# Performance work log

Hardware: AMD Instinct MI355X
Metric: run time of the kernel (lower is better)

## Reference

```python
import jax, jax.numpy as jnp
import numpy as np
import math

NINP = 1024
NOUT = 1024
NSLOTS = 15
B = 4096


def setup_inputs() -> dict:
    key = jax.random.key(0)
    ks = jax.random.split(key, 10)
    inp = {
        "input": jax.random.normal(ks[0], (B, NINP), jnp.float32),
        "gate_time": jax.random.uniform(ks[1], (B, NSLOTS), jnp.float32),
        "rmask": jnp.ones((B, NOUT), jnp.float32),
        "memory_h": jax.random.normal(ks[2], (B, NSLOTS, NOUT), jnp.float32),
        "memory_c": jax.random.normal(ks[3], (B, NSLOTS, NOUT), jnp.float32),
        # projector_summ: Linear(ninp+nout, nout) (dropouts are identity in eval)
        "W_proj": jax.random.normal(ks[4], (NOUT, NINP + NOUT), jnp.float32) / np.sqrt(NINP + NOUT),
        "b_proj": jnp.zeros((NOUT,), jnp.float32),
        # LSTMCell(ninp, nout) weights, torch gate order [i, f, g, o]
        "W_ih": jax.random.normal(ks[5], (4 * NOUT, NINP), jnp.float32) / np.sqrt(NINP),
        "W_hh": jax.random.normal(ks[6], (4 * NOUT, NOUT), jnp.float32) / np.sqrt(NOUT),
        "b_ih": jnp.zeros((4 * NOUT,), jnp.float32),
        "b_hh": jnp.zeros((4 * NOUT,), jnp.float32),
    }
    return inp


def reference(input, gate_time, rmask, memory_h, memory_c,
              W_proj, b_proj, W_ih, W_hh, b_ih, b_hh):
    # --- attention over memory slots (gated softmax) ---
    key = jnp.concatenate([input, memory_h[:, 0, :]], axis=1) @ W_proj.T + b_proj  # [B, nout]
    logits = jnp.einsum('bsd,bd->bs', memory_h, key) / math.sqrt(NOUT)             # [B, nslots]
    e = jnp.exp(logits - jnp.max(logits, axis=1, keepdims=True)) * gate_time
    attention = e / jnp.sum(e, axis=1, keepdims=True)
    sel_h = jnp.einsum('bs,bsd->bd', attention, memory_h)
    sel_c = jnp.einsum('bs,bsd->bd', attention, memory_c)

    # --- LSTM cell step (dropout = identity in eval) ---
    gates = input @ W_ih.T + b_ih + (sel_h * rmask) @ W_hh.T + b_hh
    i, f, g, o = jnp.split(gates, 4, axis=1)
    c_i = jax.nn.sigmoid(f) * sel_c + jax.nn.sigmoid(i) * jnp.tanh(g)
    h_i = jax.nn.sigmoid(o) * jnp.tanh(c_i)

    # --- rolling memory update: push new state to slot 0 ---
    memory_h_new = jnp.concatenate([h_i[:, None, :], memory_h[:, :-1, :]], axis=1)
    memory_c_new = jnp.concatenate([c_i[:, None, :], memory_c[:, :-1, :]], axis=1)
    return h_i, memory_h_new, memory_c_new, attention
```

## Files before the change

kernel.cpp:

```cpp
#include <hip/hip_runtime.h>

typedef __attribute__((ext_vector_type(8))) __bf16 bf16x8;
typedef __attribute__((ext_vector_type(4))) float f32x4;
typedef unsigned short u16;
typedef unsigned int u32;

#define NINP 1024
#define NOUT 1024
#define NSLOTS 15
#define BB 4096

__device__ __forceinline__ u16 f2bf(float x) {
  u32 u = __float_as_uint(x);
  u = (u + 0x7FFFu + ((u >> 16) & 1u)) >> 16;
  return (u16)u;
}
__device__ __forceinline__ float bf2f(u16 u) {
  return __uint_as_float(((u32)u) << 16);
}
__device__ __forceinline__ float sigf(float x) {
  return 1.0f / (1.0f + __expf(-x));
}
__device__ __forceinline__ float tanhfast(float x) {
  return 1.0f - 2.0f / (__expf(2.0f * x) + 1.0f);
}

__device__ __forceinline__ void llds16(const u16* g, const u16* l) {
  __builtin_amdgcn_global_load_lds(
      (const __attribute__((address_space(1))) void*)g,
      (__attribute__((address_space(3))) void*)l, 16, 0, 0);
}

__global__ void convert_kernel(const float* __restrict__ input,
                               const float* __restrict__ mem_h,
                               const float* __restrict__ W_proj,
                               const float* __restrict__ W_ih,
                               const float* __restrict__ W_hh,
                               u16* __restrict__ X2, u16* __restrict__ WP,
                               u16* __restrict__ WG) {
  const int S0 = 4194304, S1 = 4194304, S2 = 2097152, S3 = 4194304, S4 = 4194304;
  const int total4 = (S0 + S1 + S2 + S3 + S4) >> 2;
  for (int i4 = blockIdx.x * blockDim.x + threadIdx.x; i4 < total4;
       i4 += gridDim.x * blockDim.x) {
    int i = i4 << 2;
    const float* src;
    u16* dst;
    if (i < S0) {
      int j = i, b = j >> 10, d = j & 1023;
      src = input + j;
      dst = X2 + ((size_t)b << 11) + d;
    } else if (i < S0 + S1) {
      int j = i - S0, b = j >> 10, d = j & 1023;
      src = mem_h + (size_t)b * (NSLOTS * NOUT) + d;
      dst = X2 + ((size_t)b << 11) + 1024 + d;
    } else if (i < S0 + S1 + S2) {
      int j = i - S0 - S1;
      src = W_proj + j;
      dst = WP + j;
    } else if (i < S0 + S1 + S2 + S3) {
      int j = i - S0 - S1 - S2, n = j >> 10, k = j & 1023;
      src = W_ih + j;
      dst = WG + ((size_t)n << 11) + k;
    } else {
      int j = i - S0 - S1 - S2 - S3, n = j >> 10, k = j & 1023;
      src = W_hh + j;
      dst = WG + ((size_t)n << 11) + 1024 + k;
    }
    float4 v = *(const float4*)src;
    ushort4 o;
    o.x = f2bf(v.x); o.y = f2bf(v.y); o.z = f2bf(v.z); o.w = f2bf(v.w);
    *(ushort4*)dst = o;
  }
}

__global__ __launch_bounds__(256) void gemm_bt(
    const u16* __restrict__ A, const u16* __restrict__ W,
    const float* __restrict__ bias1, const float* __restrict__ bias2,
    float* __restrict__ Cf, u16* __restrict__ Cb, int M, int N, int K) {
  __shared__ u16 sA[2][128 * 32];
  __shared__ u16 sB[2][128 * 32];
  const int t = threadIdx.x;
  const int wave = t >> 6, lane = t & 63;
  const int m0 = blockIdx.y * 128, n0 = blockIdx.x * 128;
  const int wr = (wave >> 1) * 64, wc = (wave & 1) * 64;

  f32x4 acc[4][4] = {};

  const int row0 = t >> 2, col0 = (t & 3) * 8;
  const int row1 = (t + 256) >> 2;
  const u16* Ag0 = A + (size_t)(m0 + row0) * K + col0;
  const u16* Ag1 = A + (size_t)(m0 + row1) * K + col0;
  const u16* Wg0 = W + (size_t)(n0 + row0) * K + col0;
  const u16* Wg1 = W + (size_t)(n0 + row1) * K + col0;
  const int l0 = (wave * 64) * 8;
  const int l1 = (256 + wave * 64) * 8;

  auto stage = [&](int buf, int kt) {
    const int k0 = kt * 32;
    llds16(Ag0 + k0, &sA[buf][l0]);
    llds16(Ag1 + k0, &sA[buf][l1]);
    llds16(Wg0 + k0, &sB[buf][l0]);
    llds16(Wg1 + k0, &sB[buf][l1]);
  };

  const int lrow = lane & 15;
  const int kq = (lane >> 4) * 8;

  const int nk = K / 32;
  stage(0, 0);
  for (int kt = 0; kt < nk; ++kt) {
    __syncthreads();
    if (kt + 1 < nk) stage((kt + 1) & 1, kt + 1);
    const int buf = kt & 1;
    bf16x8 af[4], bfr[4];
#pragma unroll
    for (int mi = 0; mi < 4; ++mi)
      af[mi] = *(const bf16x8*)&sA[buf][(wr + mi * 16 + lrow) * 32 + kq];
#pragma unroll
    for (int ni = 0; ni < 4; ++ni)
      bfr[ni] = *(const bf16x8*)&sB[buf][(wc + ni * 16 + lrow) * 32 + kq];
#pragma unroll
    for (int mi = 0; mi < 4; ++mi)
#pragma unroll
      for (int ni = 0; ni < 4; ++ni)
        acc[mi][ni] = __builtin_amdgcn_mfma_f32_16x16x32_bf16(
            af[mi], bfr[ni], acc[mi][ni], 0, 0, 0);
  }

  const int crow = (lane >> 4) * 4;
  const int ccol = lane & 15;
#pragma unroll
  for (int mi = 0; mi < 4; ++mi) {
#pragma unroll
    for (int ni = 0; ni < 4; ++ni) {
      int row = m0 + wr + mi * 16 + crow;
      int col = n0 + wc + ni * 16 + ccol;
      float bv = bias1 ? bias1[col] : 0.0f;
      if (bias2) bv += bias2[col];
#pragma unroll
      for (int r = 0; r < 4; ++r) {
        float v = acc[mi][ni][r] + bv;
        if (Cb)
          Cb[(size_t)(row + r) * N + col] = f2bf(v);
        else
          Cf[(size_t)(row + r) * N + col] = v;
      }
    }
  }
}

__global__ __launch_bounds__(512, 2) void gemm256(
    const u16* __restrict__ A, const u16* __restrict__ W,
    const float* __restrict__ bias1, const float* __restrict__ bias2,
    u16* __restrict__ Cb, int M, int N, int K) {
  extern __shared__ __align__(16) u16 smem[];
  u16* sA = smem;
  u16* sB = smem + 32768;

  const int t = threadIdx.x;
  const int wid = t >> 6, lane = t & 63;
  const int nbx = N >> 8;
  const int nb = (M >> 8) * nbx;
  const int cpx = nb >> 3;
  const int bid = blockIdx.x;
  const int wg = (bid & 7) * cpx + (bid >> 3);
  const int m0 = (wg / nbx) << 8;
  const int n0 = (wg % nbx) << 8;

  const int wm = wid >> 2, wn = wid & 3;

  f32x4 acc[8][4] = {};

  const int src_swz = ((lane >> 5) & 1) << 4;
  const u16* gA[4];
  const u16* gB[4];
#pragma unroll
  for (int j = 0; j < 4; ++j) {
    int row = (j & 1) * 128 + (t >> 2);
    int col = (j >> 1) * 32 + ((((t & 3) * 8) ^ src_swz));
    gA[j] = A + (size_t)(m0 + row) * K + col;
    gB[j] = W + (size_t)(n0 + row) * K + col;
  }
  auto stage = [&](int kt, int buf) {
    const int ko = kt * 64;
    const int lb = buf * 16384;
#pragma unroll
    for (int j = 0; j < 4; ++j)
      llds16(gA[j] + ko, sA + lb + (j * 512 + wid * 64) * 8);
#pragma unroll
    for (int j = 0; j < 4; ++j)
      llds16(gB[j] + ko, sB + lb + (j * 512 + wid * 64) * 8);
  };

  const int lrow = lane & 15;
  const int lcol = ((lane >> 4) * 8) ^ (((lane >> 3) & 1) << 4);
  const u16* pA = sA + (wm * 128 + lrow) * 32 + lcol;
  const u16* pB = sB + (wn * 64 + lrow) * 32 + lcol;

  const int NKT = K >> 6;
  stage(0, 0);
  for (int kt = 0; kt < NKT; ++kt) {
    const int buf = kt & 1;
    if (kt + 1 < NKT) {
      stage(kt + 1, buf ^ 1);
      asm volatile("s_waitcnt vmcnt(8)" ::: "memory");
      __builtin_amdgcn_sched_barrier(0);
    } else {
      asm volatile("s_waitcnt vmcnt(0)" ::: "memory");
      __builtin_amdgcn_sched_barrier(0);
    }
    __builtin_amdgcn_s_barrier();

    const u16* bA = pA + buf * 16384;
    const u16* bB = pB + buf * 16384;

    bf16x8 bf[4][2];
#pragma unroll
    for (int ni = 0; ni < 4; ++ni)
#pragma unroll
      for (int ks = 0; ks < 2; ++ks)
        bf[ni][ks] = *(const bf16x8*)(bB + ks * 8192 + ni * (16 * 32));

#pragma unroll
    for (int ph = 0; ph < 4; ++ph) {
      bf16x8 af[2][2];
#pragma unroll
      for (int m2 = 0; m2 < 2; ++m2)
#pragma unroll
        for (int ks = 0; ks < 2; ++ks)
          af[m2][ks] =
              *(const bf16x8*)(bA + ks * 8192 + (ph * 2 + m2) * (16 * 32));
      __builtin_amdgcn_s_setprio(1);
#pragma unroll
      for (int ks = 0; ks < 2; ++ks)
#pragma unroll
        for (int m2 = 0; m2 < 2; ++m2)
#pragma unroll
          for (int ni = 0; ni < 4; ++ni)
            acc[ph * 2 + m2][ni] = __builtin_amdgcn_mfma_f32_16x16x32_bf16(
                af[m2][ks], bf[ni][ks], acc[ph * 2 + m2][ni], 0, 0, 0);
      __builtin_amdgcn_s_setprio(0);
      __builtin_amdgcn_s_barrier();
    }
  }

  const int crow = (lane >> 4) * 4;
  const int ccol = lane & 15;
#pragma unroll
  for (int mi = 0; mi < 8; ++mi) {
#pragma unroll
    for (int ni = 0; ni < 4; ++ni) {
      int row = m0 + wm * 128 + mi * 16 + crow;
      int col = n0 + wn * 64 + ni * 16 + ccol;
      float bv = bias1[col] + bias2[col];
#pragma unroll
      for (int r = 0; r < 4; ++r)
        Cb[(size_t)(row + r) * N + col] = f2bf(acc[mi][ni][r] + bv);
    }
  }
}

__global__ __launch_bounds__(256) void attn_kernel(
    const float* __restrict__ mem_h, const float* __restrict__ mem_c,
    const float* __restrict__ key, const float* __restrict__ gate_time,
    const float* __restrict__ rmask, float* __restrict__ out_mh,
    float* __restrict__ out_mc, float* __restrict__ out_att,
    u16* __restrict__ X2, float* __restrict__ selc) {
  const int b = blockIdx.x;
  const int t = threadIdx.x;
  const int lane = t & 63, wave = t >> 6;

  const float4* mh4 = (const float4*)(mem_h + (size_t)b * (NSLOTS * NOUT));
  const float4* mc4 = (const float4*)(mem_c + (size_t)b * (NSLOTS * NOUT));
  float4 key4 = ((const float4*)(key + ((size_t)b << 10)))[t];

  float4 h[NSLOTS];
  float lg[NSLOTS];
#pragma unroll
  for (int s = 0; s < NSLOTS; ++s) {
    h[s] = mh4[s * 256 + t];
    lg[s] = h[s].x * key4.x + h[s].y * key4.y + h[s].z * key4.z + h[s].w * key4.w;
  }

  __shared__ float red[NSLOTS][4];
#pragma unroll
  for (int s = 0; s < NSLOTS; ++s) {
    float v = lg[s];
    v += __shfl_xor(v, 32); v += __shfl_xor(v, 16); v += __shfl_xor(v, 8);
    v += __shfl_xor(v, 4);  v += __shfl_xor(v, 2);  v += __shfl_xor(v, 1);
    if (lane == 0) red[s][wave] = v;
  }
  __syncthreads();

  float att[NSLOTS];
  float mx = -1e30f;
#pragma unroll
  for (int s = 0; s < NSLOTS; ++s) {
    float v = red[s][0] + red[s][1] + red[s][2] + red[s][3];
    att[s] = v * 0.03125f;
    mx = fmaxf(mx, att[s]);
  }
  float ssum = 0.0f;
#pragma unroll
  for (int s = 0; s < NSLOTS; ++s) {
    att[s] = __expf(att[s] - mx) * gate_time[b * NSLOTS + s];
    ssum += att[s];
  }
  float inv = 1.0f / ssum;
#pragma unroll
  for (int s = 0; s < NSLOTS; ++s) att[s] *= inv;
  if (t == 0) {
#pragma unroll
    for (int s = 0; s < NSLOTS; ++s) out_att[(size_t)b * NSLOTS + s] = att[s];
  }

  float4 sh = {0, 0, 0, 0};
  float4* omh = (float4*)(out_mh + (size_t)b * (NSLOTS * NOUT));
#pragma unroll
  for (int s = 0; s < NSLOTS; ++s) {
    sh.x += att[s] * h[s].x; sh.y += att[s] * h[s].y;
    sh.z += att[s] * h[s].z; sh.w += att[s] * h[s].w;
    if (s < NSLOTS - 1) omh[(s + 1) * 256 + t] = h[s];
  }
  float4 rm = ((const float4*)(rmask + ((size_t)b << 10)))[t];
  sh.x *= rm.x; sh.y *= rm.y; sh.z *= rm.z; sh.w *= rm.w;
  ushort4 shb;
  shb.x = f2bf(sh.x); shb.y = f2bf(sh.y); shb.z = f2bf(sh.z); shb.w = f2bf(sh.w);
  ((ushort4*)(X2 + ((size_t)b << 11) + 1024))[t] = shb;

  float4 sc = {0, 0, 0, 0};
  float4* omc = (float4*)(out_mc + (size_t)b * (NSLOTS * NOUT));
#pragma unroll
  for (int s = 0; s < NSLOTS; ++s) {
    float4 c = mc4[s * 256 + t];
    sc.x += att[s] * c.x; sc.y += att[s] * c.y;
    sc.z += att[s] * c.z; sc.w += att[s] * c.w;
    if (s < NSLOTS - 1) omc[(s + 1) * 256 + t] = c;
  }
  ((float4*)(selc + ((size_t)b << 10)))[t] = sc;
}

__global__ __launch_bounds__(256) void lstm_ew(const u16* __restrict__ gates,
                                               const float* __restrict__ selc,
                                               float* __restrict__ out_h,
                                               float* __restrict__ out_mh,
                                               float* __restrict__ out_mc) {
  int gid = blockIdx.x * blockDim.x + threadIdx.x;
  int b = gid >> 8, t = gid & 255;
  const ushort4* g = (const ushort4*)(gates + ((size_t)b << 12));
  ushort4 iu = g[t], fu = g[256 + t], gu = g[512 + t], ou = g[768 + t];
  float4 sc = ((const float4*)(selc + ((size_t)b << 10)))[t];

  float4 cv, hv;
  {
    float i0 = sigf(bf2f(iu.x)), f0 = sigf(bf2f(fu.x));
    float g0 = tanhfast(bf2f(gu.x)), o0 = sigf(bf2f(ou.x));
    cv.x = f0 * sc.x + i0 * g0; hv.x = o0 * tanhfast(cv.x);
  }
  {
    float i0 = sigf(bf2f(iu.y)), f0 = sigf(bf2f(fu.y));
    float g0 = tanhfast(bf2f(gu.y)), o0 = sigf(bf2f(ou.y));
    cv.y = f0 * sc.y + i0 * g0; hv.y = o0 * tanhfast(cv.y);
  }
  {
    float i0 = sigf(bf2f(iu.z)), f0 = sigf(bf2f(fu.z));
    float g0 = tanhfast(bf2f(gu.z)), o0 = sigf(bf2f(ou.z));
    cv.z = f0 * sc.z + i0 * g0; hv.z = o0 * tanhfast(cv.z);
  }
  {
    float i0 = sigf(bf2f(iu.w)), f0 = sigf(bf2f(fu.w));
    float g0 = tanhfast(bf2f(gu.w)), o0 = sigf(bf2f(ou.w));
    cv.w = f0 * sc.w + i0 * g0; hv.w = o0 * tanhfast(cv.w);
  }
  ((float4*)(out_h + ((size_t)b << 10)))[t] = hv;
  ((float4*)(out_mh + (size_t)b * (NSLOTS * NOUT)))[t] = hv;
  ((float4*)(out_mc + (size_t)b * (NSLOTS * NOUT)))[t] = cv;
}

extern "C" void kernel_launch(void* const* d_in, const int* in_sizes, int n_in,
                              void* d_out, int out_size, void* d_ws,
                              size_t ws_size, hipStream_t stream) {
  const float* input = (const float*)d_in[0];
  const float* gate_time = (const float*)d_in[1];
  const float* rmask = (const float*)d_in[2];
  const float* mem_h = (const float*)d_in[3];
  const float* mem_c = (const float*)d_in[4];
  const float* W_proj = (const float*)d_in[5];
  const float* b_proj = (const float*)d_in[6];
  const float* W_ih = (const float*)d_in[7];
  const float* W_hh = (const float*)d_in[8];
  const float* b_ih = (const float*)d_in[9];
  const float* b_hh = (const float*)d_in[10];

  float* out = (float*)d_out;
  float* out_h = out;
  float* out_mh = out + 4194304;
  float* out_mc = out_mh + 62914560;
  float* out_att = out_mc + 62914560;

  char* ws = (char*)d_ws;
  u16* X2 = (u16*)ws;
  u16* WP = (u16*)(ws + 16777216);
  u16* WG = (u16*)(ws + 20971520);
  float* key = (float*)(ws + 37748736);
  float* selc = (float*)(ws + 54525952);
  u16* gates = (u16*)(ws + 71303168);

  (void)hipFuncSetAttribute((const void*)gemm256,
                            hipFuncAttributeMaxDynamicSharedMemorySize, 131072);

  convert_kernel<<<2048, 256, 0, stream>>>(input, mem_h, W_proj, W_ih, W_hh, X2,
                                           WP, WG);
  gemm_bt<<<dim3(8, 32), 256, 0, stream>>>(X2, WP, b_proj, nullptr, key,
                                           nullptr, 4096, 1024, 2048);
  attn_kernel<<<4096, 256, 0, stream>>>(mem_h, mem_c, key, gate_time, rmask,
                                        out_mh, out_mc, out_att, X2, selc);
  gemm256<<<256, 512, 131072, stream>>>(X2, WG, b_ih, b_hh, gates, 4096, 4096,
                                        2048);
  lstm_ew<<<4096, 256, 0, stream>>>(gates, selc, out_h, out_mh, out_mc);
}
```

Before: 368.9 us.

## Fuse LSTM elementwise into gate GEMM epilogue with interleaved gate weight rows

Weight rows for the four LSTM gates are interleaved during conversion, so each 256-wide GEMM output tile holds all four gates for 64 hidden units. The GEMM epilogue stages accumulators through shared memory and computes the LSTM cell directly, writing h and c. This removes the bf16 gates buffer round trip and the separate lstm_ew launch. The projection GEMM also writes its key output in bf16 instead of fp32, which halves that traffic but adds rounding error to the attention logits.

```diff
diff --git a/kernel.cpp b/kernel.cpp
--- a/kernel.cpp
+++ b/kernel.cpp
@@ -59,12 +59,14 @@
       dst = WP + j;
     } else if (i < S0 + S1 + S2 + S3) {
       int j = i - S0 - S1 - S2, n = j >> 10, k = j & 1023;
+      int gate = n >> 10, d = n & 1023;
       src = W_ih + j;
-      dst = WG + ((size_t)n << 11) + k;
+      dst = WG + ((size_t)((d << 2) | gate) << 11) + k;
     } else {
       int j = i - S0 - S1 - S2 - S3, n = j >> 10, k = j & 1023;
+      int gate = n >> 10, d = n & 1023;
       src = W_hh + j;
-      dst = WG + ((size_t)n << 11) + 1024 + k;
+      dst = WG + ((size_t)((d << 2) | gate) << 11) + 1024 + k;
     }
     float4 v = *(const float4*)src;
     ushort4 o;
@@ -75,8 +77,8 @@
 
 __global__ __launch_bounds__(256) void gemm_bt(
     const u16* __restrict__ A, const u16* __restrict__ W,
-    const float* __restrict__ bias1, const float* __restrict__ bias2,
-    float* __restrict__ Cf, u16* __restrict__ Cb, int M, int N, int K) {
+    const float* __restrict__ bias1, u16* __restrict__ Cb, int M, int N,
+    int K) {
   __shared__ u16 sA[2][128 * 32];
   __shared__ u16 sB[2][128 * 32];
   const int t = threadIdx.x;
@@ -136,23 +138,19 @@
       int row = m0 + wr + mi * 16 + crow;
       int col = n0 + wc + ni * 16 + ccol;
       float bv = bias1 ? bias1[col] : 0.0f;
-      if (bias2) bv += bias2[col];
-#pragma unroll
-      for (int r = 0; r < 4; ++r) {
-        float v = acc[mi][ni][r] + bv;
-        if (Cb)
-          Cb[(size_t)(row + r) * N + col] = f2bf(v);
-        else
-          Cf[(size_t)(row + r) * N + col] = v;
-      }
-    }
-  }
-}
-
-__global__ __launch_bounds__(512, 2) void gemm256(
+#pragma unroll
+      for (int r = 0; r < 4; ++r)
+        Cb[(size_t)(row + r) * N + col] = f2bf(acc[mi][ni][r] + bv);
+    }
+  }
+}
+
+__global__ __launch_bounds__(512, 2) void gemm256_lstm(
     const u16* __restrict__ A, const u16* __restrict__ W,
-    const float* __restrict__ bias1, const float* __restrict__ bias2,
-    u16* __restrict__ Cb, int M, int N, int K) {
+    const float* __restrict__ b_ih, const float* __restrict__ b_hh,
+    const float* __restrict__ selc, float* __restrict__ out_h,
+    float* __restrict__ out_mh, float* __restrict__ out_mc, int M, int N,
+    int K) {
   extern __shared__ __align__(16) u16 smem[];
   u16* sA = smem;
   u16* sB = smem + 32768;
@@ -244,25 +242,64 @@
     }
   }
 
+  float* slab = (float*)smem;
   const int crow = (lane >> 4) * 4;
   const int ccol = lane & 15;
-#pragma unroll
+  const int d0 = n0 >> 2;
+
+  __builtin_amdgcn_s_barrier();
+#pragma unroll 1
   for (int mi = 0; mi < 8; ++mi) {
 #pragma unroll
     for (int ni = 0; ni < 4; ++ni) {
-      int row = m0 + wm * 128 + mi * 16 + crow;
-      int col = n0 + wn * 64 + ni * 16 + ccol;
-      float bv = bias1[col] + bias2[col];
+      int c = wn * 64 + ni * 16 + ccol;
+      int g = c & 3, dl = c >> 2;
 #pragma unroll
       for (int r = 0; r < 4; ++r)
-        Cb[(size_t)(row + r) * N + col] = f2bf(acc[mi][ni][r] + bv);
-    }
+        slab[wm * 4352 + (crow + r) * 272 + g * 68 + dl] = acc[mi][ni][r];
+    }
+    __builtin_amdgcn_s_barrier();
+    {
+      const int row_id = t >> 4;
+      const int slabi = row_id >> 4, rr = row_id & 15;
+      const int k4 = (t & 15) * 4;
+      const int grow = m0 + slabi * 128 + mi * 16 + rr;
+      const int gd = d0 + k4;
+      f32x4 gv[4];
+#pragma unroll
+      for (int g = 0; g < 4; ++g) {
+        f32x4 v = *(const f32x4*)&slab[slabi * 4352 + rr * 272 + g * 68 + k4];
+        float4 b1 = *(const float4*)&b_ih[(g << 10) + gd];
+        float4 b2 = *(const float4*)&b_hh[(g << 10) + gd];
+        gv[g][0] = v[0] + b1.x + b2.x;
+        gv[g][1] = v[1] + b1.y + b2.y;
+        gv[g][2] = v[2] + b1.z + b2.z;
+        gv[g][3] = v[3] + b1.w + b2.w;
+      }
+      float4 sc = *(const float4*)&selc[(size_t)grow * 1024 + gd];
+      float scv[4] = {sc.x, sc.y, sc.z, sc.w};
+      float4 cv, hv;
+      float cvv[4], hvv[4];
+#pragma unroll
+      for (int j = 0; j < 4; ++j) {
+        float ii = sigf(gv[0][j]), ff = sigf(gv[1][j]);
+        float gg = tanhfast(gv[2][j]), oo = sigf(gv[3][j]);
+        cvv[j] = ff * scv[j] + ii * gg;
+        hvv[j] = oo * tanhfast(cvv[j]);
+      }
+      cv.x = cvv[0]; cv.y = cvv[1]; cv.z = cvv[2]; cv.w = cvv[3];
+      hv.x = hvv[0]; hv.y = hvv[1]; hv.z = hvv[2]; hv.w = hvv[3];
+      *(float4*)&out_h[(size_t)grow * 1024 + gd] = hv;
+      *(float4*)&out_mh[(size_t)grow * (NSLOTS * NOUT) + gd] = hv;
+      *(float4*)&out_mc[(size_t)grow * (NSLOTS * NOUT) + gd] = cv;
+    }
+    __builtin_amdgcn_s_barrier();
   }
 }
 
 __global__ __launch_bounds__(256) void attn_kernel(
     const float* __restrict__ mem_h, const float* __restrict__ mem_c,
-    const float* __restrict__ key, const float* __restrict__ gate_time,
+    const u16* __restrict__ keyb, const float* __restrict__ gate_time,
     const float* __restrict__ rmask, float* __restrict__ out_mh,
     float* __restrict__ out_mc, float* __restrict__ out_att,
     u16* __restrict__ X2, float* __restrict__ selc) {
@@ -272,7 +309,8 @@
 
   const float4* mh4 = (const float4*)(mem_h + (size_t)b * (NSLOTS * NOUT));
   const float4* mc4 = (const float4*)(mem_c + (size_t)b * (NSLOTS * NOUT));
-  float4 key4 = ((const float4*)(key + ((size_t)b << 10)))[t];
+  ushort4 kb = ((const ushort4*)(keyb + ((size_t)b << 10)))[t];
+  float4 key4 = {bf2f(kb.x), bf2f(kb.y), bf2f(kb.z), bf2f(kb.w)};
 
   float4 h[NSLOTS];
   float lg[NSLOTS];
@@ -338,43 +376,6 @@
     if (s < NSLOTS - 1) omc[(s + 1) * 256 + t] = c;
   }
   ((float4*)(selc + ((size_t)b << 10)))[t] = sc;
-}
-
-__global__ __launch_bounds__(256) void lstm_ew(const u16* __restrict__ gates,
-                                               const float* __restrict__ selc,
-                                               float* __restrict__ out_h,
-                                               float* __restrict__ out_mh,
-                                               float* __restrict__ out_mc) {
-  int gid = blockIdx.x * blockDim.x + threadIdx.x;
-  int b = gid >> 8, t = gid & 255;
-  const ushort4* g = (const ushort4*)(gates + ((size_t)b << 12));
-  ushort4 iu = g[t], fu = g[256 + t], gu = g[512 + t], ou = g[768 + t];
-  float4 sc = ((const float4*)(selc + ((size_t)b << 10)))[t];
-
-  float4 cv, hv;
-  {
-    float i0 = sigf(bf2f(iu.x)), f0 = sigf(bf2f(fu.x));
-    float g0 = tanhfast(bf2f(gu.x)), o0 = sigf(bf2f(ou.x));
-    cv.x = f0 * sc.x + i0 * g0; hv.x = o0 * tanhfast(cv.x);
-  }
-  {
-    float i0 = sigf(bf2f(iu.y)), f0 = sigf(bf2f(fu.y));
-    float g0 = tanhfast(bf2f(gu.y)), o0 = sigf(bf2f(ou.y));
-    cv.y = f0 * sc.y + i0 * g0; hv.y = o0 * tanhfast(cv.y);
-  }
-  {
-    float i0 = sigf(bf2f(iu.z)), f0 = sigf(bf2f(fu.z));
-    float g0 = tanhfast(bf2f(gu.z)), o0 = sigf(bf2f(ou.z));
-    cv.z = f0 * sc.z + i0 * g0; hv.z = o0 * tanhfast(cv.z);
-  }
-  {
-    float i0 = sigf(bf2f(iu.w)), f0 = sigf(bf2f(fu.w));
-    float g0 = tanhfast(bf2f(gu.w)), o0 = sigf(bf2f(ou.w));
-    cv.w = f0 * sc.w + i0 * g0; hv.w = o0 * tanhfast(cv.w);
-  }
-  ((float4*)(out_h + ((size_t)b << 10)))[t] = hv;
-  ((float4*)(out_mh + (size_t)b * (NSLOTS * NOUT)))[t] = hv;
-  ((float4*)(out_mc + (size_t)b * (NSLOTS * NOUT)))[t] = cv;
 }
 
 extern "C" void kernel_launch(void* const* d_in, const int* in_sizes, int n_in,
@@ -402,20 +403,18 @@
   u16* X2 = (u16*)ws;
   u16* WP = (u16*)(ws + 16777216);
   u16* WG = (u16*)(ws + 20971520);
-  float* key = (float*)(ws + 37748736);
-  float* selc = (float*)(ws + 54525952);
-  u16* gates = (u16*)(ws + 71303168);
-
-  (void)hipFuncSetAttribute((const void*)gemm256,
+  u16* keyb = (u16*)(ws + 37748736);
+  float* selc = (float*)(ws + 46137344);
+
+  (void)hipFuncSetAttribute((const void*)gemm256_lstm,
                             hipFuncAttributeMaxDynamicSharedMemorySize, 131072);
 
   convert_kernel<<<2048, 256, 0, stream>>>(input, mem_h, W_proj, W_ih, W_hh, X2,
                                            WP, WG);
-  gemm_bt<<<dim3(8, 32), 256, 0, stream>>>(X2, WP, b_proj, nullptr, key,
-                                           nullptr, 4096, 1024, 2048);
-  attn_kernel<<<4096, 256, 0, stream>>>(mem_h, mem_c, key, gate_time, rmask,
+  gemm_bt<<<dim3(8, 32), 256, 0, stream>>>(X2, WP, b_proj, keyb, 4096, 1024,
+                                           2048);
+  attn_kernel<<<4096, 256, 0, stream>>>(mem_h, mem_c, keyb, gate_time, rmask,
                                         out_mh, out_mc, out_att, X2, selc);
-  gemm256<<<256, 512, 131072, stream>>>(X2, WG, b_ih, b_hh, gates, 4096, 4096,
-                                        2048);
-  lstm_ew<<<4096, 256, 0, stream>>>(gates, selc, out_h, out_mh, out_mc);
-}
+  gemm256_lstm<<<256, 512, 131072, stream>>>(X2, WG, b_ih, b_hh, selc, out_h,
+                                             out_mh, out_mc, 4096, 4096, 2048);
+}
```

After: 384.8 us. +4.3%, slower.

## Store key and selected cell state in bf16, use nontemporal streaming memory ops

Applied to the files above, without the earlier changes.

The projection GEMM now writes its key output in bf16 instead of fp32, and the attention kernel writes the attention-weighted cell state (selc) in bf16. This halves those intermediate buffers. The large memory_h/memory_c reads and shifted-slot writes switch to nontemporal loads and stores to avoid polluting cache, and the LSTM elementwise kernel processes 8 elements per thread with nontemporal stores. Keeping key and sel_c in bf16 adds precision loss to the logits and the cell-state path, which may hurt output accuracy.

```diff
diff --git a/kernel.cpp b/kernel.cpp
--- a/kernel.cpp
+++ b/kernel.cpp
@@ -2,6 +2,7 @@
 
 typedef __attribute__((ext_vector_type(8))) __bf16 bf16x8;
 typedef __attribute__((ext_vector_type(4))) float f32x4;
+typedef __attribute__((ext_vector_type(8))) unsigned short u16x8;
 typedef unsigned short u16;
 typedef unsigned int u32;
 
@@ -66,17 +67,17 @@
       src = W_hh + j;
       dst = WG + ((size_t)n << 11) + 1024 + k;
     }
-    float4 v = *(const float4*)src;
+    f32x4 v = *(const f32x4*)src;
     ushort4 o;
-    o.x = f2bf(v.x); o.y = f2bf(v.y); o.z = f2bf(v.z); o.w = f2bf(v.w);
+    o.x = f2bf(v[0]); o.y = f2bf(v[1]); o.z = f2bf(v[2]); o.w = f2bf(v[3]);
     *(ushort4*)dst = o;
   }
 }
 
 __global__ __launch_bounds__(256) void gemm_bt(
     const u16* __restrict__ A, const u16* __restrict__ W,
-    const float* __restrict__ bias1, const float* __restrict__ bias2,
-    float* __restrict__ Cf, u16* __restrict__ Cb, int M, int N, int K) {
+    const float* __restrict__ bias1, u16* __restrict__ Cb, int M, int N,
+    int K) {
   __shared__ u16 sA[2][128 * 32];
   __shared__ u16 sB[2][128 * 32];
   const int t = threadIdx.x;
@@ -136,15 +137,9 @@
       int row = m0 + wr + mi * 16 + crow;
       int col = n0 + wc + ni * 16 + ccol;
       float bv = bias1 ? bias1[col] : 0.0f;
-      if (bias2) bv += bias2[col];
-#pragma unroll
-      for (int r = 0; r < 4; ++r) {
-        float v = acc[mi][ni][r] + bv;
-        if (Cb)
-          Cb[(size_t)(row + r) * N + col] = f2bf(v);
-        else
-          Cf[(size_t)(row + r) * N + col] = v;
-      }
+#pragma unroll
+      for (int r = 0; r < 4; ++r)
+        Cb[(size_t)(row + r) * N + col] = f2bf(acc[mi][ni][r] + bv);
     }
   }
 }
@@ -262,24 +257,26 @@
 
 __global__ __launch_bounds__(256) void attn_kernel(
     const float* __restrict__ mem_h, const float* __restrict__ mem_c,
-    const float* __restrict__ key, const float* __restrict__ gate_time,
+    const u16* __restrict__ keyb, const float* __restrict__ gate_time,
     const float* __restrict__ rmask, float* __restrict__ out_mh,
     float* __restrict__ out_mc, float* __restrict__ out_att,
-    u16* __restrict__ X2, float* __restrict__ selc) {
+    u16* __restrict__ X2, u16* __restrict__ selcb) {
   const int b = blockIdx.x;
   const int t = threadIdx.x;
   const int lane = t & 63, wave = t >> 6;
 
-  const float4* mh4 = (const float4*)(mem_h + (size_t)b * (NSLOTS * NOUT));
-  const float4* mc4 = (const float4*)(mem_c + (size_t)b * (NSLOTS * NOUT));
-  float4 key4 = ((const float4*)(key + ((size_t)b << 10)))[t];
-
-  float4 h[NSLOTS];
+  const f32x4* mh4 = (const f32x4*)(mem_h + (size_t)b * (NSLOTS * NOUT));
+  const f32x4* mc4 = (const f32x4*)(mem_c + (size_t)b * (NSLOTS * NOUT));
+  ushort4 kb = ((const ushort4*)(keyb + ((size_t)b << 10)))[t];
+  f32x4 key4 = {bf2f(kb.x), bf2f(kb.y), bf2f(kb.z), bf2f(kb.w)};
+
+  f32x4 h[NSLOTS];
   float lg[NSLOTS];
 #pragma unroll
   for (int s = 0; s < NSLOTS; ++s) {
-    h[s] = mh4[s * 256 + t];
-    lg[s] = h[s].x * key4.x + h[s].y * key4.y + h[s].z * key4.z + h[s].w * key4.w;
+    h[s] = __builtin_nontemporal_load(&mh4[s * 256 + t]);
+    lg[s] = h[s][0] * key4[0] + h[s][1] * key4[1] + h[s][2] * key4[2] +
+            h[s][3] * key4[3];
   }
 
   __shared__ float red[NSLOTS][4];
@@ -314,67 +311,72 @@
     for (int s = 0; s < NSLOTS; ++s) out_att[(size_t)b * NSLOTS + s] = att[s];
   }
 
-  float4 sh = {0, 0, 0, 0};
-  float4* omh = (float4*)(out_mh + (size_t)b * (NSLOTS * NOUT));
-#pragma unroll
-  for (int s = 0; s < NSLOTS; ++s) {
-    sh.x += att[s] * h[s].x; sh.y += att[s] * h[s].y;
-    sh.z += att[s] * h[s].z; sh.w += att[s] * h[s].w;
-    if (s < NSLOTS - 1) omh[(s + 1) * 256 + t] = h[s];
-  }
-  float4 rm = ((const float4*)(rmask + ((size_t)b << 10)))[t];
-  sh.x *= rm.x; sh.y *= rm.y; sh.z *= rm.z; sh.w *= rm.w;
+  f32x4 sh = {0, 0, 0, 0};
+  f32x4* omh = (f32x4*)(out_mh + (size_t)b * (NSLOTS * NOUT));
+#pragma unroll
+  for (int s = 0; s < NSLOTS; ++s) {
+    sh += att[s] * h[s];
+    if (s < NSLOTS - 1)
+      __builtin_nontemporal_store(h[s], &omh[(s + 1) * 256 + t]);
+  }
+  f32x4 rm = *(const f32x4*)(rmask + ((size_t)b << 10) + t * 4);
+  sh *= rm;
   ushort4 shb;
-  shb.x = f2bf(sh.x); shb.y = f2bf(sh.y); shb.z = f2bf(sh.z); shb.w = f2bf(sh.w);
+  shb.x = f2bf(sh[0]); shb.y = f2bf(sh[1]);
+  shb.z = f2bf(sh[2]); shb.w = f2bf(sh[3]);
   ((ushort4*)(X2 + ((size_t)b << 11) + 1024))[t] = shb;
 
-  float4 sc = {0, 0, 0, 0};
-  float4* omc = (float4*)(out_mc + (size_t)b * (NSLOTS * NOUT));
-#pragma unroll
-  for (int s = 0; s < NSLOTS; ++s) {
-    float4 c = mc4[s * 256 + t];
-    sc.x += att[s] * c.x; sc.y += att[s] * c.y;
-    sc.z += att[s] * c.z; sc.w += att[s] * c.w;
-    if (s < NSLOTS - 1) omc[(s + 1) * 256 + t] = c;
-  }
-  ((float4*)(selc + ((size_t)b << 10)))[t] = sc;
+  f32x4 sc = {0, 0, 0, 0};
+  f32x4* omc = (f32x4*)(out_mc + (size_t)b * (NSLOTS * NOUT));
+#pragma unroll
+  for (int s = 0; s < NSLOTS; ++s) {
+    f32x4 c = __builtin_nontemporal_load(&mc4[s * 256 + t]);
+    sc += att[s] * c;
+    if (s < NSLOTS - 1)
+      __builtin_nontemporal_store(c, &omc[(s + 1) * 256 + t]);
+  }
+  ushort4 scb;
+  scb.x = f2bf(sc[0]); scb.y = f2bf(sc[1]);
+  scb.z = f2bf(sc[2]); scb.w = f2bf(sc[3]);
+  ((ushort4*)(selcb + ((size_t)b << 10)))[t] = scb;
 }
 
 __global__ __launch_bounds__(256) void lstm_ew(const u16* __restrict__ gates,
-                                               const float* __restrict__ selc,
+                                               const u16* __restrict__ selcb,
                                                float* __restrict__ out_h,
                                                float* __restrict__ out_mh,
                                                float* __restrict__ out_mc) {
   int gid = blockIdx.x * blockDim.x + threadIdx.x;
-  int b = gid >> 8, t = gid & 255;
-  const ushort4* g = (const ushort4*)(gates + ((size_t)b << 12));
-  ushort4 iu = g[t], fu = g[256 + t], gu = g[512 + t], ou = g[768 + t];
-  float4 sc = ((const float4*)(selc + ((size_t)b << 10)))[t];
-
-  float4 cv, hv;
-  {
-    float i0 = sigf(bf2f(iu.x)), f0 = sigf(bf2f(fu.x));
-    float g0 = tanhfast(bf2f(gu.x)), o0 = sigf(bf2f(ou.x));
-    cv.x = f0 * sc.x + i0 * g0; hv.x = o0 * tanhfast(cv.x);
-  }
-  {
-    float i0 = sigf(bf2f(iu.y)), f0 = sigf(bf2f(fu.y));
-    float g0 = tanhfast(bf2f(gu.y)), o0 = sigf(bf2f(ou.y));
-    cv.y = f0 * sc.y + i0 * g0; hv.y = o0 * tanhfast(cv.y);
-  }
-  {
-    float i0 = sigf(bf2f(iu.z)), f0 = sigf(bf2f(fu.z));
-    float g0 = tanhfast(bf2f(gu.z)), o0 = sigf(bf2f(ou.z));
-    cv.z = f0 * sc.z + i0 * g0; hv.z = o0 * tanhfast(cv.z);
-  }
-  {
-    float i0 = sigf(bf2f(iu.w)), f0 = sigf(bf2f(fu.w));
-    float g0 = tanhfast(bf2f(gu.w)), o0 = sigf(bf2f(ou.w));
-    cv.w = f0 * sc.w + i0 * g0; hv.w = o0 * tanhfast(cv.w);
-  }
-  ((float4*)(out_h + ((size_t)b << 10)))[t] = hv;
-  ((float4*)(out_mh + (size_t)b * (NSLOTS * NOUT)))[t] = hv;
-  ((float4*)(out_mc + (size_t)b * (NSLOTS * NOUT)))[t] = cv;
+  int b = gid >> 7, d8 = (gid & 127) << 3;
+  const u16* gbase = gates + ((size_t)b << 12) + d8;
+  u16x8 iu = *(const u16x8*)(gbase);
+  u16x8 fu = *(const u16x8*)(gbase + 1024);
+  u16x8 gu = *(const u16x8*)(gbase + 2048);
+  u16x8 ou = *(const u16x8*)(gbase + 3072);
+  u16x8 su = *(const u16x8*)(selcb + ((size_t)b << 10) + d8);
+
+  float hv[8], cvv[8];
+#pragma unroll
+  for (int j = 0; j < 8; ++j) {
+    float ii = sigf(bf2f(iu[j])), ff = sigf(bf2f(fu[j]));
+    float gg = tanhfast(bf2f(gu[j])), oo = sigf(bf2f(ou[j]));
+    float sc = bf2f(su[j]);
+    cvv[j] = ff * sc + ii * gg;
+    hv[j] = oo * tanhfast(cvv[j]);
+  }
+  f32x4 h0 = {hv[0], hv[1], hv[2], hv[3]};
+  f32x4 h1 = {hv[4], hv[5], hv[6], hv[7]};
+  f32x4 c0 = {cvv[0], cvv[1], cvv[2], cvv[3]};
+  f32x4 c1 = {cvv[4], cvv[5], cvv[6], cvv[7]};
+  float* oh = out_h + ((size_t)b << 10) + d8;
+  float* omh = out_mh + (size_t)b * (NSLOTS * NOUT) + d8;
+  float* omc = out_mc + (size_t)b * (NSLOTS * NOUT) + d8;
+  __builtin_nontemporal_store(h0, (f32x4*)oh);
+  __builtin_nontemporal_store(h1, (f32x4*)(oh + 4));
+  __builtin_nontemporal_store(h0, (f32x4*)omh);
+  __builtin_nontemporal_store(h1, (f32x4*)(omh + 4));
+  __builtin_nontemporal_store(c0, (f32x4*)omc);
+  __builtin_nontemporal_store(c1, (f32x4*)(omc + 4));
 }
 
 extern "C" void kernel_launch(void* const* d_in, const int* in_sizes, int n_in,
@@ -402,20 +404,20 @@
   u16* X2 = (u16*)ws;
   u16* WP = (u16*)(ws + 16777216);
   u16* WG = (u16*)(ws + 20971520);
-  float* key = (float*)(ws + 37748736);
-  float* selc = (float*)(ws + 54525952);
-  u16* gates = (u16*)(ws + 71303168);
+  u16* keyb = (u16*)(ws + 37748736);
+  u16* selcb = (u16*)(ws + 46137344);
+  u16* gates = (u16*)(ws + 54525952);
 
   (void)hipFuncSetAttribute((const void*)gemm256,
                             hipFuncAttributeMaxDynamicSharedMemorySize, 131072);
 
   convert_kernel<<<2048, 256, 0, stream>>>(input, mem_h, W_proj, W_ih, W_hh, X2,
                                            WP, WG);
-  gemm_bt<<<dim3(8, 32), 256, 0, stream>>>(X2, WP, b_proj, nullptr, key,
-                                           nullptr, 4096, 1024, 2048);
-  attn_kernel<<<4096, 256, 0, stream>>>(mem_h, mem_c, key, gate_time, rmask,
-                                        out_mh, out_mc, out_att, X2, selc);
+  gemm_bt<<<dim3(8, 32), 256, 0, stream>>>(X2, WP, b_proj, keyb, 4096, 1024,
+                                           2048);
+  attn_kernel<<<4096, 256, 0, stream>>>(mem_h, mem_c, keyb, gate_time, rmask,
+                                        out_mh, out_mc, out_att, X2, selcb);
   gemm256<<<256, 512, 131072, stream>>>(X2, WG, b_ih, b_hh, gates, 4096, 4096,
                                         2048);
-  lstm_ew<<<4096, 256, 0, stream>>>(gates, selc, out_h, out_mh, out_mc);
-}
+  lstm_ew<<<2048, 256, 0, stream>>>(gates, selcb, out_h, out_mh, out_mc);
+}
```

Measured after the change: 330.7 us. -10.3%, faster.
